# Performance work log

Measured on AMD Instinct MI355X. Metric: run time of the kernel, lower is better.

## Reference

```python
import jax, jax.numpy as jnp
import numpy as np
import math

B, S, HID = 1, 2048, 4096
NH, NKV, HD = 32, 8, 128
N_REP = NH // NKV
ROPE_THETA = 10000.0


def setup_inputs() -> dict:
    key = jax.random.key(0)
    ks = jax.random.split(key, 5)
    hidden_states = jax.random.normal(ks[0], (B, S, HID), dtype=jnp.float32)
    # additive causal mask: 0 on/below diagonal, -1e9 above
    causal = jnp.triu(jnp.full((S, S), -1e9, dtype=jnp.float32), k=1)
    attention_mask = causal[None, None, :, :]
    wq = jax.random.normal(ks[1], (HID, NH * HD), dtype=jnp.float32) * 0.02
    wk = jax.random.normal(ks[2], (HID, NKV * HD), dtype=jnp.float32) * 0.02
    wv = jax.random.normal(ks[3], (HID, NKV * HD), dtype=jnp.float32) * 0.02
    wo = jax.random.normal(ks[4], (NH * HD, HID), dtype=jnp.float32) * 0.02
    return {"hidden_states": hidden_states, "attention_mask": attention_mask,
            "wq": wq, "wk": wk, "wv": wv, "wo": wo}


def _rope_cos_sin(seq_len, head_dim, base, dtype):
    inv_freq = 1.0 / (base ** (jnp.arange(0, head_dim, 2, dtype=jnp.float32) / head_dim))
    t = jnp.arange(seq_len, dtype=jnp.float32)
    freqs = jnp.outer(t, inv_freq)          # [S, HD/2]
    emb = jnp.concatenate([freqs, freqs], axis=-1)  # [S, HD]
    return jnp.cos(emb).astype(dtype), jnp.sin(emb).astype(dtype)


def _rotate_interleaved(x):
    # pairs (x0,x1) -> (-x1, x0), interleaved (matches torch stack/reshape trick)
    xp = x.reshape(*x.shape[:-1], -1, 2)
    return jnp.stack([-xp[..., 1], xp[..., 0]], axis=-1).reshape(x.shape)


def reference(hidden_states, attention_mask, wq, wk, wv, wo):
    b, s, _ = hidden_states.shape
    q = (hidden_states @ wq).reshape(b, s, NH, HD).transpose(0, 2, 1, 3)   # [B,NH,S,HD]
    k = (hidden_states @ wk).reshape(b, s, NKV, HD).transpose(0, 2, 1, 3)  # [B,NKV,S,HD]
    v = (hidden_states @ wv).reshape(b, s, NKV, HD).transpose(0, 2, 1, 3)

    cos, sin = _rope_cos_sin(s, HD, ROPE_THETA, hidden_states.dtype)
    cos = cos[None, None, :, :]  # broadcast over batch and heads
    sin = sin[None, None, :, :]
    q = q * cos + _rotate_interleaved(q) * sin
    k = k * cos + _rotate_interleaved(k) * sin

    # repeat_kv: [B,NKV,S,HD] -> [B,NH,S,HD]
    k = jnp.repeat(k, N_REP, axis=1)
    v = jnp.repeat(v, N_REP, axis=1)

    scores = jnp.einsum('bhqd,bhkd->bhqk', q, k) / math.sqrt(HD)
    scores = scores + attention_mask
    attn = jax.nn.softmax(scores.astype(jnp.float32), axis=-1).astype(q.dtype)
    out = jnp.einsum('bhqk,bhkd->bhqd', attn, v)          # [B,NH,S,HD]
    out = out.transpose(0, 2, 1, 3).reshape(b, s, NH * HD)
    return out @ wo
```

## Files before the change

kernel.cpp:

```cpp
#include <hip/hip_runtime.h>

#define S_LEN 2048
#define HID 4096
#define NH 32
#define NKV 8
#define HD 128
#define KVW 1024
#define NQKV 6144

typedef _Float16 f16;
typedef _Float16 f16x8 __attribute__((ext_vector_type(8)));
typedef _Float16 f16x4 __attribute__((ext_vector_type(4)));
typedef float f32x4 __attribute__((ext_vector_type(4)));
typedef float f32x16 __attribute__((ext_vector_type(16)));
typedef unsigned int u32;
typedef u32 u32x4 __attribute__((ext_vector_type(4)));

__device__ __forceinline__ void gll16(const void* g, void* lds) {
  __builtin_amdgcn_global_load_lds((const __attribute__((address_space(1))) void*)g,
                                   (__attribute__((address_space(3))) void*)lds, 16, 0, 0);
}

__global__ void k_cast(const float* __restrict__ src, f16* __restrict__ dst) {
  size_t i = ((size_t)blockIdx.x * blockDim.x + threadIdx.x) * 8;
  float4 a = *(const float4*)(src + i);
  float4 b = *(const float4*)(src + i + 4);
  f16x8 o = { (f16)a.x, (f16)a.y, (f16)a.z, (f16)a.w,
              (f16)b.x, (f16)b.y, (f16)b.z, (f16)b.w };
  *(f16x8*)(dst + i) = o;
}

__global__ void k_trig(float4* __restrict__ trig) {
  int id = blockIdx.x * blockDim.x + threadIdx.x;
  int s = id >> 6, i = id & 63;
  int j0 = 2 * i, j1 = 2 * i + 1;
  float f0 = powf(10000.f, -(float)(j0 & 63) / 64.f);
  float f1 = powf(10000.f, -(float)(j1 & 63) / 64.f);
  float a0 = (float)s * f0, a1 = (float)s * f1;
  trig[id] = make_float4(cosf(a0), cosf(a1), sinf(a0), sinf(a1));
}

__global__ void k_transpose(const float* __restrict__ src, f16* __restrict__ dst, int N) {
  __shared__ f16 tile[64][72];
  int nb = blockIdx.x * 64, kb = blockIdx.y * 64;
  int t = threadIdx.x;
  int kl = t >> 4, nc = (t & 15) << 2;
#pragma unroll
  for (int p = 0; p < 4; ++p) {
    int kk = kl + p * 16;
    float4 v = *(const float4*)(src + (size_t)(kb + kk) * N + nb + nc);
    f16x4 h = { (f16)v.x, (f16)v.y, (f16)v.z, (f16)v.w };
    *(f16x4*)(&tile[kk][nc]) = h;
  }
  __syncthreads();
  int nl = t >> 3, c = t & 7;
#pragma unroll
  for (int p = 0; p < 2; ++p) {
    int nn = nl + p * 32;
    f16x8 o;
#pragma unroll
    for (int i = 0; i < 8; ++i) o[i] = tile[c * 8 + i][nn];
    *(f16x8*)(dst + (size_t)(nb + nn) * HID + kb + c * 8) = o;
  }
}

#define BM 128
#define BN 128
#define BK 64

template<int MODE>
__global__ __launch_bounds__(256, 4) void k_gemm(
    const f16* __restrict__ A, const f16* __restrict__ Bt,
    int N, int K,
    f16* __restrict__ Qr, f16* __restrict__ Kr, f16* __restrict__ Vt,
    const float4* __restrict__ trig, float* __restrict__ Cout)
{
  __shared__ f16 As[BM * BK];
  __shared__ f16 Bs[BN * BK];
  const int tid = threadIdx.x;
  const int ln = tid & 63, w = tid >> 6;
  const int la = ln & 15, lg = ln >> 4;
  const int m0 = blockIdx.y * BM, n0 = blockIdx.x * BN;
  const int NT = K / BK;

  f32x4 acc[4][4] = {};

  size_t aoff[4], boff[4];
  int ldsc[4];
#pragma unroll
  for (int j = 0; j < 4; ++j) {
    int cch = w * 4 + j;
    int r = cch * 8 + (ln >> 3);
    int gc = (ln & 7) ^ (r & 7);
    aoff[j] = ((size_t)(m0 + r) * K) * 2 + (size_t)gc * 16;
    boff[j] = ((size_t)(n0 + r) * K) * 2 + (size_t)gc * 16;
    ldsc[j] = cch * 1024;
  }

  const int wm = (w & 1) * 64, wn = (w >> 1) * 64;
  int arow[4], brow[4];
#pragma unroll
  for (int i = 0; i < 4; ++i) { arow[i] = wm + i * 16 + la; brow[i] = wn + i * 16 + la; }

  for (int kt = 0; kt < NT; ++kt) {
    const char* Ab = (const char*)A + (size_t)kt * BK * 2;
    const char* Bb = (const char*)Bt + (size_t)kt * BK * 2;
#pragma unroll
    for (int j = 0; j < 4; ++j) {
      gll16(Ab + aoff[j], (char*)&As[0] + ldsc[j]);
      gll16(Bb + boff[j], (char*)&Bs[0] + ldsc[j]);
    }
    __syncthreads();
    f16x8 af[4][2], bf[4][2];
#pragma unroll
    for (int i = 0; i < 4; ++i) {
#pragma unroll
      for (int ks = 0; ks < 2; ++ks) {
        int ca = (ks * 4 + lg) ^ (arow[i] & 7);
        int cb = (ks * 4 + lg) ^ (brow[i] & 7);
        af[i][ks] = *(const f16x8*)(As + arow[i] * 64 + ca * 8);
        bf[i][ks] = *(const f16x8*)(Bs + brow[i] * 64 + cb * 8);
      }
    }
#pragma unroll
    for (int mi = 0; mi < 4; ++mi)
#pragma unroll
      for (int ni = 0; ni < 4; ++ni)
#pragma unroll
        for (int ks = 0; ks < 2; ++ks)
          acc[mi][ni] = __builtin_amdgcn_mfma_f32_16x16x32_f16(af[mi][ks], bf[ni][ks], acc[mi][ni], 0, 0, 0);
    __syncthreads();
  }

#pragma unroll
  for (int mi = 0; mi < 4; ++mi) {
#pragma unroll
    for (int ni = 0; ni < 4; ++ni) {
      f32x4 fr = acc[mi][ni];
      int n = n0 + wn + ni * 16 + la;
      int mr = m0 + wm + mi * 16 + lg * 4;
      if (MODE == 0) {
        if (n < HID + KVW) {
          int d = n & 127;
#pragma unroll
          for (int r = 0; r < 4; ++r) {
            float v = fr[r];
            float p = __shfl_xor(v, 1);
            float4 tc = trig[(size_t)(mr + r) * 64 + (d >> 1)];
            float cv = (d & 1) ? tc.y : tc.x;
            float sv = (d & 1) ? tc.w : tc.z;
            float o = v * cv + ((d & 1) ? p : -p) * sv;
            if (n < HID) Qr[(size_t)(mr + r) * HID + n] = (f16)o;
            else         Kr[(size_t)(mr + r) * KVW + (n - HID)] = (f16)o;
          }
        } else {
          int nv = n - (HID + KVW);
          f16x4 o4 = { (f16)fr[0], (f16)fr[1], (f16)fr[2], (f16)fr[3] };
          *(f16x4*)(Vt + (size_t)nv * S_LEN + mr) = o4;
        }
      } else {
#pragma unroll
        for (int r = 0; r < 4; ++r)
          Cout[(size_t)(mr + r) * N + n] = fr[r];
      }
    }
  }
}

#define KBYTES (64 * 128 * 2)
#define VBYTES (128 * 64 * 2)

__global__ __launch_bounds__(256, 2) void k_attn(
    const f16* __restrict__ Qr, const f16* __restrict__ Kr, const f16* __restrict__ Vt,
    f16* __restrict__ AO)
{
  int bid = blockIdx.x;
  int h, c;
  if (bid < 256) { h = bid >> 3; c = bid & 7; }
  else           { int t = bid - 256; h = t >> 3; c = 15 - (t & 7); }
  const int hkv = h >> 2;
  const int q0c = c * 128;
  const int NT = 2 * c + 2;

  __shared__ char KV[2][KBYTES + VBYTES];

  const int tid = threadIdx.x;
  const int ln = tid & 63, w = tid >> 6;
  const int q = ln & 31;
  const int hi = ln >> 5;
  const int qg = q0c + w * 32 + q;

  size_t ksrc[4], vsrc[4];
  int kdo[4], vdo[4];
#pragma unroll
  for (int j = 0; j < 4; ++j) {
    int kc = w * 4 + j;
    int kr = kc * 4 + (ln >> 4);
    ksrc[j] = ((size_t)kr * KVW + hkv * HD) * 2 + (size_t)(((ln & 15) ^ (kr & 7)) * 16);
    kdo[j] = kc * 1024;
    int vc = w * 4 + j;
    int d = vc * 8 + (ln >> 3);
    vsrc[j] = ((size_t)(hkv * HD + d) * S_LEN) * 2 + (size_t)(((ln & 7) ^ (d & 7)) * 16);
    vdo[j] = KBYTES + vc * 1024;
  }

  f16x8 qf[8];
  {
    const f16* qrow = Qr + (size_t)qg * HID + h * HD + hi * 8;
#pragma unroll
    for (int ks = 0; ks < 8; ++ks) qf[ks] = *(const f16x8*)(qrow + ks * 16);
  }

  f32x16 ot[4] = {};
  float m2 = -3.0e38f, l = 0.f;
  const float K2 = 0.12753256471f;

  int buf = 0;
#pragma unroll
  for (int j = 0; j < 4; ++j) {
    gll16((const char*)Kr + ksrc[j], &KV[0][kdo[j]]);
    gll16((const char*)Vt + vsrc[j], &KV[0][vdo[j]]);
  }

  for (int jt = 0; jt < NT; ++jt) {
    __syncthreads();
    if (jt + 1 < NT) {
      size_t ko = (size_t)(jt + 1) * 64 * KVW * 2;
      size_t vo = (size_t)(jt + 1) * 64 * 2;
#pragma unroll
      for (int j = 0; j < 4; ++j) {
        gll16((const char*)Kr + ksrc[j] + ko, &KV[buf ^ 1][kdo[j]]);
        gll16((const char*)Vt + vsrc[j] + vo, &KV[buf ^ 1][vdo[j]]);
      }
    }
    const int j0 = jt * 64;
    if (j0 <= q0c + w * 32 + 31) {
      const f16* Kb = (const f16*)&KV[buf][0];
      const f16* Vb = (const f16*)&KV[buf][KBYTES];
      f32x16 s0 = {}, s1 = {};
#pragma unroll
      for (int ks = 0; ks < 8; ++ks) {
        int cc = ((ks * 2 + hi) ^ (q & 7)) * 8;
        f16x8 k0 = *(const f16x8*)(Kb + q * 128 + cc);
        f16x8 k1 = *(const f16x8*)(Kb + (q + 32) * 128 + cc);
        s0 = __builtin_amdgcn_mfma_f32_32x32x16_f16(k0, qf[ks], s0, 0, 0, 0);
        s1 = __builtin_amdgcn_mfma_f32_32x32x16_f16(k1, qf[ks], s1, 0, 0, 0);
      }
      const bool nm = (j0 + 63 > q0c + w * 32);
      float p0[16], p1[16];
      float mx = -3.0e38f;
#pragma unroll
      for (int r = 0; r < 16; ++r) {
        float a = s0[r], b = s1[r];
        if (nm) {
          int kvb = j0 + (r & 3) + 8 * (r >> 2) + 4 * hi;
          if (kvb > qg) a = -3.0e38f;
          if (kvb + 32 > qg) b = -3.0e38f;
        }
        p0[r] = a; p1[r] = b;
        mx = fmaxf(mx, fmaxf(a, b));
      }
      mx = fmaxf(mx, __shfl_xor(mx, 32));
      float m2c = mx * K2;
      int defer = (m2c <= m2 + 11.0f);
      if (!__all(defer)) {
        float m2n = fmaxf(m2, m2c);
        float corr = exp2f(m2 - m2n);
        m2 = m2n; l *= corr;
#pragma unroll
        for (int t = 0; t < 4; ++t)
#pragma unroll
          for (int r = 0; r < 16; ++r) ot[t][r] *= corr;
      }
      float sum = 0.f;
#pragma unroll
      for (int r = 0; r < 16; ++r) {
        p0[r] = exp2f(__builtin_fmaf(p0[r], K2, -m2));
        p1[r] = exp2f(__builtin_fmaf(p1[r], K2, -m2));
        sum += p0[r] + p1[r];
      }
      l += sum + __shfl_xor(sum, 32);
      u32 pw0[8], pw1[8];
#pragma unroll
      for (int t = 0; t < 8; ++t) {
        pw0[t] = __builtin_bit_cast(u32, __builtin_amdgcn_cvt_pkrtz(p0[2 * t], p0[2 * t + 1]));
        pw1[t] = __builtin_bit_cast(u32, __builtin_amdgcn_cvt_pkrtz(p1[2 * t], p1[2 * t + 1]));
      }
      f16x8 pf[4];
#pragma unroll
      for (int ch = 0; ch < 2; ++ch) {
        const u32* pw = ch ? pw1 : pw0;
        u32 sx[8];
#pragma unroll
        for (int t = 0; t < 8; ++t) sx[t] = (u32)__shfl_xor((int)pw[t], 32);
        u32x4 fa = { hi ? sx[2] : pw[0], hi ? sx[3] : pw[1],
                     hi ? pw[2] : sx[0], hi ? pw[3] : sx[1] };
        u32x4 fb = { hi ? sx[6] : pw[4], hi ? sx[7] : pw[5],
                     hi ? pw[6] : sx[4], hi ? pw[7] : sx[5] };
        pf[ch * 2 + 0] = __builtin_bit_cast(f16x8, fa);
        pf[ch * 2 + 1] = __builtin_bit_cast(f16x8, fb);
      }
#pragma unroll
      for (int dt = 0; dt < 4; ++dt) {
        int d = dt * 32 + q;
#pragma unroll
        for (int f = 0; f < 4; ++f) {
          f16x8 vf = *(const f16x8*)(Vb + d * 64 + (((f * 2 + hi) ^ (q & 7)) * 8));
          ot[dt] = __builtin_amdgcn_mfma_f32_32x32x16_f16(vf, pf[f], ot[dt], 0, 0, 0);
        }
      }
    }
    buf ^= 1;
  }

  __syncthreads();
  char* scr = &KV[0][0] + w * 8192;
  float inv = 1.f / l;
#pragma unroll
  for (int dt = 0; dt < 4; ++dt) {
#pragma unroll
    for (int rg = 0; rg < 4; ++rg) {
      u32 wa = __builtin_bit_cast(u32, __builtin_amdgcn_cvt_pkrtz(ot[dt][rg * 4 + 0] * inv, ot[dt][rg * 4 + 1] * inv));
      u32 wb = __builtin_bit_cast(u32, __builtin_amdgcn_cvt_pkrtz(ot[dt][rg * 4 + 2] * inv, ot[dt][rg * 4 + 3] * inv));
      int byte = q * 256 + (((dt * 4 + rg) ^ (q & 7)) * 16) + hi * 8;
      u32* p = (u32*)(scr + byte);
      p[0] = wa; p[1] = wb;
    }
  }
  asm volatile("s_waitcnt lgkmcnt(0)" ::: "memory");
#pragma unroll
  for (int ps = 0; ps < 8; ++ps) {
    int qr = ps * 4 + (ln >> 4);
    int ck = (ln & 15) ^ (qr & 7);
    f16x8 v = *(const f16x8*)(scr + qr * 256 + ck * 16);
    *(f16x8*)(AO + (size_t)(q0c + w * 32 + qr) * HID + h * HD + (ln & 15) * 8) = v;
  }
}

extern "C" void kernel_launch(void* const* d_in, const int* in_sizes, int n_in,
                              void* d_out, int out_size, void* d_ws, size_t ws_size,
                              hipStream_t stream) {
  const float* hs = (const float*)d_in[0];
  const float* wq = (const float*)d_in[2];
  const float* wk = (const float*)d_in[3];
  const float* wv = (const float*)d_in[4];
  const float* wo = (const float*)d_in[5];
  float* out = (float*)d_out;

  char* ws = (char*)d_ws;
  size_t off = 0;
  auto alloc = [&](size_t b) { char* p = ws + off; off += (b + 255) & ~(size_t)255; return p; };
  f16* Hh   = (f16*)alloc((size_t)S_LEN * HID * 2);
  f16* Wt   = (f16*)alloc((size_t)NQKV * HID * 2);
  f16* Wot  = (f16*)alloc((size_t)HID * HID * 2);
  float4* trig = (float4*)alloc((size_t)S_LEN * 64 * sizeof(float4));
  f16* Qrp  = (f16*)alloc((size_t)S_LEN * HID * 2);
  f16* Krp  = (f16*)alloc((size_t)S_LEN * KVW * 2);
  f16* Vtp  = (f16*)alloc((size_t)KVW * S_LEN * 2);
  f16* AO   = (f16*)alloc((size_t)S_LEN * HID * 2);

  k_cast<<<(S_LEN * HID) / (256 * 8), 256, 0, stream>>>(hs, Hh);
  k_trig<<<(S_LEN * 64) / 256, 256, 0, stream>>>(trig);
  k_transpose<<<dim3(HID / 64, HID / 64), 256, 0, stream>>>(wq, Wt, HID);
  k_transpose<<<dim3(KVW / 64, HID / 64), 256, 0, stream>>>(wk, Wt + (size_t)HID * HID, KVW);
  k_transpose<<<dim3(KVW / 64, HID / 64), 256, 0, stream>>>(wv, Wt + (size_t)(HID + KVW) * HID, KVW);
  k_transpose<<<dim3(HID / 64, HID / 64), 256, 0, stream>>>(wo, Wot, HID);
  k_gemm<0><<<dim3(NQKV / BN, S_LEN / BM), 256, 0, stream>>>(Hh, Wt, NQKV, HID, Qrp, Krp, Vtp, trig, nullptr);
  k_attn<<<dim3(512), 256, 0, stream>>>(Qrp, Krp, Vtp, AO);
  k_gemm<1><<<dim3(HID / BN, S_LEN / BM), 256, 0, stream>>>(AO, Wot, HID, HID, nullptr, nullptr, nullptr, nullptr, out);
}
```

Before: 356.5 us.

## Rewrite GEMMs with 256-row tiles, 4-slot LDS pipeline and split-K out-projection

Replaces the 128x128 GEMM with a 512-thread kernel that computes 256-row tiles (192 or 256 columns wide). It stages K in 32-element slices through a 4-slot, 128KB dynamic-LDS ring, prefetches two slices ahead using fine-grained vmcnt waits, and raises wave priority around the MFMA block. The output projection is split along K into two halves, and a new reduce kernel sums the fp32 partials. The partials reuse the workspace that held the now-dead cast input and QKV weights. The aims are more data reuse per block, better overlap of global loads with MFMA, and a grid that fills the CUs in one wave. The costs are an unswizzled LDS layout that may cause bank conflicts, occupancy limited by LDS, and extra partial-sum traffic.

```diff
diff --git a/kernel.cpp b/kernel.cpp
--- a/kernel.cpp
+++ b/kernel.cpp
@@ -64,81 +64,88 @@
   }
 }
 
-#define BM 128
-#define BN 128
-#define BK 64
-
-template<int MODE>
-__global__ __launch_bounds__(256, 4) void k_gemm(
-    const f16* __restrict__ A, const f16* __restrict__ Bt,
-    int N, int K,
+#define SLOT 32768
+extern __shared__ char smem[];
+
+template<int MODE, int BNW, int SPLITK>
+__global__ __launch_bounds__(512, 2) void k_gemm2(
+    const f16* __restrict__ A, const f16* __restrict__ Bt, int K,
     f16* __restrict__ Qr, f16* __restrict__ Kr, f16* __restrict__ Vt,
     const float4* __restrict__ trig, float* __restrict__ Cout)
 {
-  __shared__ f16 As[BM * BK];
-  __shared__ f16 Bs[BN * BK];
-  const int tid = threadIdx.x;
-  const int ln = tid & 63, w = tid >> 6;
+  constexpr int BN = BNW * 4;
+  constexpr int NF = BNW / 16;
+  const int tid = threadIdx.x, ln = tid & 63, w = tid >> 6;
   const int la = ln & 15, lg = ln >> 4;
-  const int m0 = blockIdx.y * BM, n0 = blockIdx.x * BN;
-  const int NT = K / BK;
-
-  f32x4 acc[4][4] = {};
-
-  size_t aoff[4], boff[4];
-  int ldsc[4];
+  const int wr = w >> 2, wc = w & 3;
+  const int m0 = blockIdx.y * 256, n0 = blockIdx.x * BN;
+  const int Ksub = K / SPLITK;
+  const int NKT = Ksub / 32;
+  const int koff = (SPLITK > 1) ? blockIdx.z * Ksub : 0;
+  float* Cp = (SPLITK > 1) ? Cout + (size_t)blockIdx.z * (size_t)S_LEN * HID : Cout;
+
+  const char* gsrc[4];
+  int ldst[4];
 #pragma unroll
   for (int j = 0; j < 4; ++j) {
-    int cch = w * 4 + j;
-    int r = cch * 8 + (ln >> 3);
-    int gc = (ln & 7) ^ (r & 7);
-    aoff[j] = ((size_t)(m0 + r) * K) * 2 + (size_t)gc * 16;
-    boff[j] = ((size_t)(n0 + r) * K) * 2 + (size_t)gc * 16;
-    ldsc[j] = cch * 1024;
-  }
-
-  const int wm = (w & 1) * 64, wn = (w >> 1) * 64;
-  int arow[4], brow[4];
-#pragma unroll
-  for (int i = 0; i < 4; ++i) { arow[i] = wm + i * 16 + la; brow[i] = wn + i * 16 + la; }
-
-  for (int kt = 0; kt < NT; ++kt) {
-    const char* Ab = (const char*)A + (size_t)kt * BK * 2;
-    const char* Bb = (const char*)Bt + (size_t)kt * BK * 2;
-#pragma unroll
-    for (int j = 0; j < 4; ++j) {
-      gll16(Ab + aoff[j], (char*)&As[0] + ldsc[j]);
-      gll16(Bb + boff[j], (char*)&Bs[0] + ldsc[j]);
-    }
-    __syncthreads();
-    f16x8 af[4][2], bf[4][2];
-#pragma unroll
-    for (int i = 0; i < 4; ++i) {
-#pragma unroll
-      for (int ks = 0; ks < 2; ++ks) {
-        int ca = (ks * 4 + lg) ^ (arow[i] & 7);
-        int cb = (ks * 4 + lg) ^ (brow[i] & 7);
-        af[i][ks] = *(const f16x8*)(As + arow[i] * 64 + ca * 8);
-        bf[i][ks] = *(const f16x8*)(Bs + brow[i] * 64 + cb * 8);
-      }
-    }
-#pragma unroll
-    for (int mi = 0; mi < 4; ++mi)
-#pragma unroll
-      for (int ni = 0; ni < 4; ++ni)
-#pragma unroll
-        for (int ks = 0; ks < 2; ++ks)
-          acc[mi][ni] = __builtin_amdgcn_mfma_f32_16x16x32_f16(af[mi][ks], bf[ni][ks], acc[mi][ni], 0, 0, 0);
-    __syncthreads();
-  }
-
-#pragma unroll
-  for (int mi = 0; mi < 4; ++mi) {
-#pragma unroll
-    for (int ni = 0; ni < 4; ++ni) {
-      f32x4 fr = acc[mi][ni];
-      int n = n0 + wn + ni * 16 + la;
-      int mr = m0 + wm + mi * 16 + lg * 4;
+    int c = w * 4 + j;
+    int rr = 16 * (c & 15) + (ln >> 2);
+    int kq = ln & 3;
+    size_t off;
+    if (c < 16) {
+      off = ((size_t)(m0 + rr) * K + koff + kq * 8) * 2;
+      gsrc[j] = (const char*)A + off;
+    } else {
+      int br = (rr >= BN) ? rr - BN : rr;
+      off = ((size_t)(n0 + br) * K + koff + kq * 8) * 2;
+      gsrc[j] = (const char*)Bt + off;
+    }
+    ldst[j] = c * 1024;
+  }
+
+  f32x4 acc[8][NF] = {};
+
+#pragma unroll
+  for (int j = 0; j < 4; ++j) gll16(gsrc[j], smem + 0 * SLOT + ldst[j]);
+#pragma unroll
+  for (int j = 0; j < 4; ++j) gll16(gsrc[j] + 64, smem + 1 * SLOT + ldst[j]);
+  asm volatile("s_waitcnt vmcnt(4)" ::: "memory");
+  __builtin_amdgcn_s_barrier();
+
+  for (int t = 0; t < NKT; ++t) {
+    if (t + 2 < NKT) {
+      char* sb = smem + ((t + 2) & 3) * SLOT;
+#pragma unroll
+      for (int j = 0; j < 4; ++j)
+        gll16(gsrc[j] + (size_t)(t + 2) * 64, sb + ldst[j]);
+    }
+    const char* sb = smem + (t & 3) * SLOT;
+    f16x8 af[8], bf[NF];
+#pragma unroll
+    for (int i = 0; i < 8; ++i)
+      af[i] = *(const f16x8*)(sb + (wr * 128 + i * 16 + la) * 64 + lg * 16);
+#pragma unroll
+    for (int n = 0; n < NF; ++n)
+      bf[n] = *(const f16x8*)(sb + 16384 + (wc * BNW + n * 16 + la) * 64 + lg * 16);
+    __builtin_amdgcn_s_setprio(1);
+#pragma unroll
+    for (int i = 0; i < 8; ++i)
+#pragma unroll
+      for (int n = 0; n < NF; ++n)
+        acc[i][n] = __builtin_amdgcn_mfma_f32_16x16x32_f16(af[i], bf[n], acc[i][n], 0, 0, 0);
+    __builtin_amdgcn_s_setprio(0);
+    if (t + 2 < NKT) asm volatile("s_waitcnt vmcnt(4)" ::: "memory");
+    else             asm volatile("s_waitcnt vmcnt(0)" ::: "memory");
+    __builtin_amdgcn_s_barrier();
+  }
+
+#pragma unroll
+  for (int mi = 0; mi < 8; ++mi) {
+#pragma unroll
+    for (int nf = 0; nf < NF; ++nf) {
+      f32x4 fr = acc[mi][nf];
+      int n = n0 + wc * BNW + nf * 16 + la;
+      int mr = m0 + wr * 128 + mi * 16 + lg * 4;
       if (MODE == 0) {
         if (n < HID + KVW) {
           int d = n & 127;
@@ -161,10 +168,19 @@
       } else {
 #pragma unroll
         for (int r = 0; r < 4; ++r)
-          Cout[(size_t)(mr + r) * N + n] = fr[r];
-      }
-    }
-  }
+          Cp[(size_t)(mr + r) * HID + n] = fr[r];
+      }
+    }
+  }
+}
+
+__global__ void k_reduce(const float* __restrict__ p0, const float* __restrict__ p1,
+                         float* __restrict__ out) {
+  size_t i = ((size_t)blockIdx.x * 256 + threadIdx.x) * 4;
+  float4 a = *(const float4*)(p0 + i);
+  float4 b = *(const float4*)(p1 + i);
+  float4 o = make_float4(a.x + b.x, a.y + b.y, a.z + b.z, a.w + b.w);
+  *(float4*)(out + i) = o;
 }
 
 #define KBYTES (64 * 128 * 2)
@@ -352,12 +368,18 @@
   auto alloc = [&](size_t b) { char* p = ws + off; off += (b + 255) & ~(size_t)255; return p; };
   f16* Hh   = (f16*)alloc((size_t)S_LEN * HID * 2);
   f16* Wt   = (f16*)alloc((size_t)NQKV * HID * 2);
-  f16* Wot  = (f16*)alloc((size_t)HID * HID * 2);
   float4* trig = (float4*)alloc((size_t)S_LEN * 64 * sizeof(float4));
   f16* Qrp  = (f16*)alloc((size_t)S_LEN * HID * 2);
   f16* Krp  = (f16*)alloc((size_t)S_LEN * KVW * 2);
   f16* Vtp  = (f16*)alloc((size_t)KVW * S_LEN * 2);
   f16* AO   = (f16*)alloc((size_t)S_LEN * HID * 2);
+  f16* Wot  = (f16*)alloc((size_t)HID * HID * 2);
+  float* Pk = (float*)ws;
+
+  hipFuncSetAttribute((const void*)k_gemm2<0, 48, 1>,
+                      hipFuncAttributeMaxDynamicSharedMemorySize, 131072);
+  hipFuncSetAttribute((const void*)k_gemm2<1, 64, 2>,
+                      hipFuncAttributeMaxDynamicSharedMemorySize, 131072);
 
   k_cast<<<(S_LEN * HID) / (256 * 8), 256, 0, stream>>>(hs, Hh);
   k_trig<<<(S_LEN * 64) / 256, 256, 0, stream>>>(trig);
@@ -365,7 +387,11 @@
   k_transpose<<<dim3(KVW / 64, HID / 64), 256, 0, stream>>>(wk, Wt + (size_t)HID * HID, KVW);
   k_transpose<<<dim3(KVW / 64, HID / 64), 256, 0, stream>>>(wv, Wt + (size_t)(HID + KVW) * HID, KVW);
   k_transpose<<<dim3(HID / 64, HID / 64), 256, 0, stream>>>(wo, Wot, HID);
-  k_gemm<0><<<dim3(NQKV / BN, S_LEN / BM), 256, 0, stream>>>(Hh, Wt, NQKV, HID, Qrp, Krp, Vtp, trig, nullptr);
+  k_gemm2<0, 48, 1><<<dim3(NQKV / 192, S_LEN / 256, 1), 512, 131072, stream>>>(
+      Hh, Wt, HID, Qrp, Krp, Vtp, trig, nullptr);
   k_attn<<<dim3(512), 256, 0, stream>>>(Qrp, Krp, Vtp, AO);
-  k_gemm<1><<<dim3(HID / BN, S_LEN / BM), 256, 0, stream>>>(AO, Wot, HID, HID, nullptr, nullptr, nullptr, nullptr, out);
-}
+  k_gemm2<1, 64, 2><<<dim3(HID / 256, S_LEN / 256, 2), 512, 131072, stream>>>(
+      AO, Wot, HID, nullptr, nullptr, nullptr, nullptr, Pk);
+  k_reduce<<<(S_LEN * HID) / (256 * 4), 256, 0, stream>>>(
+      Pk, Pk + (size_t)S_LEN * HID, out);
+}
```

New measurement: 368.1 us. +3.2%, slower.

## Pipeline GEMMs with multi-buffered LDS and larger per-GEMM tile shapes

Applied to the files above, without the earlier changes.

Replaces the single-buffered GEMM with a templated kernel that keeps A tiles double-buffered and B tiles triple-buffered in dynamic LDS. Each iteration issues the next tile loads ahead of the math and waits with explicit vmcnt counts, using a single barrier per k-step instead of two. The QKV projection now uses 256x192 tiles with 512 threads, giving a grid that fits one block per CU. The output projection keeps 128x128 tiles but gains the same pipelining. The large LDS footprint lowers occupancy and relies on hand-counted waits being correct.

```diff
diff --git a/kernel.cpp b/kernel.cpp
--- a/kernel.cpp
+++ b/kernel.cpp
@@ -19,6 +19,13 @@
 __device__ __forceinline__ void gll16(const void* g, void* lds) {
   __builtin_amdgcn_global_load_lds((const __attribute__((address_space(1))) void*)g,
                                    (__attribute__((address_space(3))) void*)lds, 16, 0, 0);
+}
+
+template<int N> __device__ __forceinline__ void vmwait() {
+  if constexpr (N == 0) asm volatile("s_waitcnt vmcnt(0)" ::: "memory");
+  else if constexpr (N == 3) asm volatile("s_waitcnt vmcnt(3)" ::: "memory");
+  else if constexpr (N == 4) asm volatile("s_waitcnt vmcnt(4)" ::: "memory");
+  else static_assert(N == 0 || N == 3 || N == 4, "add vmcnt case");
 }
 
 __global__ void k_cast(const float* __restrict__ src, f16* __restrict__ dst) {
@@ -64,81 +71,102 @@
   }
 }
 
-#define BM 128
-#define BN 128
-#define BK 64
-
-template<int MODE>
-__global__ __launch_bounds__(256, 4) void k_gemm(
+extern __shared__ char smem[];
+
+template<int MODE, int MF, int NF, int WM, int WN>
+__global__ __launch_bounds__(WM * WN * 64, 2) void k_gemm4(
     const f16* __restrict__ A, const f16* __restrict__ Bt,
-    int N, int K,
     f16* __restrict__ Qr, f16* __restrict__ Kr, f16* __restrict__ Vt,
     const float4* __restrict__ trig, float* __restrict__ Cout)
 {
-  __shared__ f16 As[BM * BK];
-  __shared__ f16 Bs[BN * BK];
-  const int tid = threadIdx.x;
-  const int ln = tid & 63, w = tid >> 6;
+  constexpr int NTHR = WM * WN * 64;
+  constexpr int BM = WM * MF * 16;
+  constexpr int BN = WN * NF * 16;
+  constexpr int ABYTES = BM * 128;
+  constexpr int BBYTES = BN * 128;
+  constexpr int RPC = NTHR / 8;
+  constexpr int ACALLS = BM / RPC;
+  constexpr int BCALLS = BN / RPC;
+  constexpr int NT = 64;
+
+  const int tid = threadIdx.x, ln = tid & 63, w = tid >> 6;
   const int la = ln & 15, lg = ln >> 4;
+  const int wr = w / WN, wc = w % WN;
   const int m0 = blockIdx.y * BM, n0 = blockIdx.x * BN;
-  const int NT = K / BK;
-
-  f32x4 acc[4][4] = {};
-
-  size_t aoff[4], boff[4];
-  int ldsc[4];
-#pragma unroll
-  for (int j = 0; j < 4; ++j) {
-    int cch = w * 4 + j;
-    int r = cch * 8 + (ln >> 3);
-    int gc = (ln & 7) ^ (r & 7);
-    aoff[j] = ((size_t)(m0 + r) * K) * 2 + (size_t)gc * 16;
-    boff[j] = ((size_t)(n0 + r) * K) * 2 + (size_t)gc * 16;
-    ldsc[j] = cch * 1024;
-  }
-
-  const int wm = (w & 1) * 64, wn = (w >> 1) * 64;
-  int arow[4], brow[4];
-#pragma unroll
-  for (int i = 0; i < 4; ++i) { arow[i] = wm + i * 16 + la; brow[i] = wn + i * 16 + la; }
-
-  for (int kt = 0; kt < NT; ++kt) {
-    const char* Ab = (const char*)A + (size_t)kt * BK * 2;
-    const char* Bb = (const char*)Bt + (size_t)kt * BK * 2;
-#pragma unroll
-    for (int j = 0; j < 4; ++j) {
-      gll16(Ab + aoff[j], (char*)&As[0] + ldsc[j]);
-      gll16(Bb + boff[j], (char*)&Bs[0] + ldsc[j]);
-    }
-    __syncthreads();
-    f16x8 af[4][2], bf[4][2];
-#pragma unroll
-    for (int i = 0; i < 4; ++i) {
-#pragma unroll
-      for (int ks = 0; ks < 2; ++ks) {
-        int ca = (ks * 4 + lg) ^ (arow[i] & 7);
-        int cb = (ks * 4 + lg) ^ (brow[i] & 7);
-        af[i][ks] = *(const f16x8*)(As + arow[i] * 64 + ca * 8);
-        bf[i][ks] = *(const f16x8*)(Bs + brow[i] * 64 + cb * 8);
-      }
-    }
-#pragma unroll
-    for (int mi = 0; mi < 4; ++mi)
-#pragma unroll
-      for (int ni = 0; ni < 4; ++ni)
-#pragma unroll
-        for (int ks = 0; ks < 2; ++ks)
-          acc[mi][ni] = __builtin_amdgcn_mfma_f32_16x16x32_f16(af[mi][ks], bf[ni][ks], acc[mi][ni], 0, 0, 0);
-    __syncthreads();
-  }
-
-#pragma unroll
-  for (int mi = 0; mi < 4; ++mi) {
-#pragma unroll
-    for (int ni = 0; ni < 4; ++ni) {
-      f32x4 fr = acc[mi][ni];
-      int n = n0 + wn + ni * 16 + la;
-      int mr = m0 + wm + mi * 16 + lg * 4;
+
+  const char* asrc[ACALLS];
+  const char* bsrc[BCALLS];
+  int adst[ACALLS > BCALLS ? ACALLS : BCALLS];
+#pragma unroll
+  for (int c = 0; c < ACALLS; ++c) {
+    int r = c * RPC + (tid >> 3);
+    int g = (tid & 7) ^ (r & 7);
+    asrc[c] = (const char*)A + ((size_t)(m0 + r) * HID + (size_t)g * 8) * 2;
+    adst[c] = c * NTHR * 16 + tid * 16;
+  }
+#pragma unroll
+  for (int c = 0; c < BCALLS; ++c) {
+    int r = c * RPC + (tid >> 3);
+    int g = (tid & 7) ^ (r & 7);
+    bsrc[c] = (const char*)Bt + ((size_t)(n0 + r) * HID + (size_t)g * 8) * 2;
+  }
+
+  char* const Bbase = smem + 2 * ABYTES;
+  f32x4 acc[MF][NF] = {};
+
+#pragma unroll
+  for (int c = 0; c < ACALLS; ++c) gll16(asrc[c], smem + adst[c]);
+#pragma unroll
+  for (int c = 0; c < BCALLS; ++c) gll16(bsrc[c], Bbase + adst[c]);
+#pragma unroll
+  for (int c = 0; c < BCALLS; ++c) gll16(bsrc[c] + 128, Bbase + BBYTES + adst[c]);
+  vmwait<BCALLS>();
+  __builtin_amdgcn_s_barrier();
+
+  for (int t = 0; t < NT; ++t) {
+    if (t + 1 < NT) {
+      char* sa = smem + ((t + 1) & 1) * ABYTES;
+#pragma unroll
+      for (int c = 0; c < ACALLS; ++c) gll16(asrc[c] + (size_t)(t + 1) * 128, sa + adst[c]);
+    }
+    if (t + 2 < NT) {
+      char* sb = Bbase + ((t + 2) % 3) * BBYTES;
+#pragma unroll
+      for (int c = 0; c < BCALLS; ++c) gll16(bsrc[c] + (size_t)(t + 2) * 128, sb + adst[c]);
+    }
+    const char* sa = smem + (t & 1) * ABYTES;
+    const char* sb = Bbase + (t % 3) * BBYTES;
+#pragma unroll
+    for (int ks = 0; ks < 2; ++ks) {
+      f16x8 af[MF], bf[NF];
+#pragma unroll
+      for (int i = 0; i < MF; ++i) {
+        int rl = wr * MF * 16 + i * 16 + la;
+        af[i] = *(const f16x8*)(sa + rl * 128 + (((ks * 4 + lg) ^ (rl & 7)) * 16));
+      }
+#pragma unroll
+      for (int n = 0; n < NF; ++n) {
+        int rb = wc * NF * 16 + n * 16 + la;
+        bf[n] = *(const f16x8*)(sb + rb * 128 + (((ks * 4 + lg) ^ (rb & 7)) * 16));
+      }
+#pragma unroll
+      for (int i = 0; i < MF; ++i)
+#pragma unroll
+        for (int n = 0; n < NF; ++n)
+          acc[i][n] = __builtin_amdgcn_mfma_f32_16x16x32_f16(af[i], bf[n], acc[i][n], 0, 0, 0);
+    }
+    if (t < NT - 2)      vmwait<BCALLS>();
+    else if (t == NT - 2) vmwait<0>();
+    if (t < NT - 1) __builtin_amdgcn_s_barrier();
+  }
+
+#pragma unroll
+  for (int mi = 0; mi < MF; ++mi) {
+#pragma unroll
+    for (int nf = 0; nf < NF; ++nf) {
+      f32x4 fr = acc[mi][nf];
+      int n = n0 + wc * NF * 16 + nf * 16 + la;
+      int mr = m0 + wr * MF * 16 + mi * 16 + lg * 4;
       if (MODE == 0) {
         if (n < HID + KVW) {
           int d = n & 127;
@@ -161,7 +189,7 @@
       } else {
 #pragma unroll
         for (int r = 0; r < 4; ++r)
-          Cout[(size_t)(mr + r) * N + n] = fr[r];
+          Cout[(size_t)(mr + r) * HID + n] = fr[r];
       }
     }
   }
@@ -352,12 +380,17 @@
   auto alloc = [&](size_t b) { char* p = ws + off; off += (b + 255) & ~(size_t)255; return p; };
   f16* Hh   = (f16*)alloc((size_t)S_LEN * HID * 2);
   f16* Wt   = (f16*)alloc((size_t)NQKV * HID * 2);
-  f16* Wot  = (f16*)alloc((size_t)HID * HID * 2);
   float4* trig = (float4*)alloc((size_t)S_LEN * 64 * sizeof(float4));
   f16* Qrp  = (f16*)alloc((size_t)S_LEN * HID * 2);
   f16* Krp  = (f16*)alloc((size_t)S_LEN * KVW * 2);
   f16* Vtp  = (f16*)alloc((size_t)KVW * S_LEN * 2);
   f16* AO   = (f16*)alloc((size_t)S_LEN * HID * 2);
+  f16* Wot  = (f16*)alloc((size_t)HID * HID * 2);
+
+  hipFuncSetAttribute((const void*)k_gemm4<0, 8, 3, 2, 4>,
+                      hipFuncAttributeMaxDynamicSharedMemorySize, 139264);
+  hipFuncSetAttribute((const void*)k_gemm4<1, 4, 4, 2, 2>,
+                      hipFuncAttributeMaxDynamicSharedMemorySize, 81920);
 
   k_cast<<<(S_LEN * HID) / (256 * 8), 256, 0, stream>>>(hs, Hh);
   k_trig<<<(S_LEN * 64) / 256, 256, 0, stream>>>(trig);
@@ -365,7 +398,9 @@
   k_transpose<<<dim3(KVW / 64, HID / 64), 256, 0, stream>>>(wk, Wt + (size_t)HID * HID, KVW);
   k_transpose<<<dim3(KVW / 64, HID / 64), 256, 0, stream>>>(wv, Wt + (size_t)(HID + KVW) * HID, KVW);
   k_transpose<<<dim3(HID / 64, HID / 64), 256, 0, stream>>>(wo, Wot, HID);
-  k_gemm<0><<<dim3(NQKV / BN, S_LEN / BM), 256, 0, stream>>>(Hh, Wt, NQKV, HID, Qrp, Krp, Vtp, trig, nullptr);
+  k_gemm4<0, 8, 3, 2, 4><<<dim3(NQKV / 192, S_LEN / 256), 512, 139264, stream>>>(
+      Hh, Wt, Qrp, Krp, Vtp, trig, nullptr);
   k_attn<<<dim3(512), 256, 0, stream>>>(Qrp, Krp, Vtp, AO);
-  k_gemm<1><<<dim3(HID / BN, S_LEN / BM), 256, 0, stream>>>(AO, Wot, HID, HID, nullptr, nullptr, nullptr, nullptr, out);
-}
+  k_gemm4<1, 4, 4, 2, 2><<<dim3(HID / 128, S_LEN / 128), 256, 81920, stream>>>(
+      AO, Wot, nullptr, nullptr, nullptr, nullptr, out);
+}
```

Result: faster. 340.1 us (-4.6%).
